# Kernel tuning notes

Hardware: AMD Instinct MI355X
Metric: run time of the kernel (lower is better)

Reference implementation:

```python
import jax, jax.numpy as jnp
import numpy as np

TOP_K = 4  # router top-k


def setup_inputs() -> dict:
    key = jax.random.key(0)
    ks = jax.random.split(key, 8)
    B, S, D, E, H, HS = 2, 2048, 2048, 16, 1024, 4096
    scaled = lambda k, shape, fan: (jax.random.normal(k, shape, jnp.float32) * (fan ** -0.5))
    return {
        "x": jax.random.normal(ks[0], (B, S, D), jnp.float32),
        "w_router": scaled(ks[1], (D, E), D),
        # per-expert SwiGLU MLP weights
        "we1": scaled(ks[2], (E, D, H), D),
        "we3": scaled(ks[3], (E, D, H), D),
        "we2": scaled(ks[4], (E, H, D), H),
        # shared SwiGLU MLP weights
        "ws1": scaled(ks[5], (D, HS), D),
        "ws3": scaled(ks[6], (D, HS), D),
        "ws2": scaled(ks[7], (HS, D), HS),
    }


def reference(x, w_router, we1, we3, we2, ws1, ws3, ws2):
    B, S, D = x.shape
    T = B * S
    E = w_router.shape[1]
    xt = x.reshape(T, D)

    # ---- router: softmax over experts, top-k, renormalize top-k weights ----
    probs = jax.nn.softmax(xt @ w_router, axis=-1)           # [T, E]
    top_w, top_i = jax.lax.top_k(probs, TOP_K)               # [T, K]
    top_w = top_w / jnp.sum(top_w, axis=-1, keepdims=True)
    # dense combine weights [T, E] (zero for non-selected experts)
    cw = jnp.zeros((T, E), xt.dtype).at[jnp.arange(T)[:, None], top_i].add(top_w)

    # ---- experts: per-expert SwiGLU, combine with routing weights ----
    g = jax.nn.silu(jnp.einsum("td,edh->teh", xt, we1)) * jnp.einsum("td,edh->teh", xt, we3)
    g = g * cw[:, :, None]                                   # fold combine weight in
    moe_out = jnp.einsum("teh,ehd->td", g, we2)              # [T, D]

    # ---- shared MLP (SwiGLU) and blend ----
    shared = (jax.nn.silu(xt @ ws1) * (xt @ ws3)) @ ws2      # [T, D]
    k = TOP_K
    out = shared / (k + 1) + moe_out * (k / (k + 1))
    return out.reshape(B, S, D)
```

## Files before the change

kernel.cpp:

```cpp
#include <hip/hip_runtime.h>
#include <stdint.h>

#define TTOK  4096
#define DDIM  2048
#define NEXP  16
#define HDIM  1024
#define HSDIM 4096
#define CAPR  18432

typedef __bf16 bf16x8 __attribute__((ext_vector_type(8)));
typedef float  f32x4  __attribute__((ext_vector_type(4)));

__device__ __forceinline__ unsigned short f2b(float f) {
  union { float f; unsigned int i; } v; v.f = f;
  unsigned int r = (v.i + 0x7fffu + ((v.i >> 16) & 1u)) >> 16;
  return (unsigned short)r;
}
__device__ __forceinline__ float b2f(unsigned short u) {
  union { unsigned int i; float f; } v; v.i = ((unsigned int)u) << 16; return v.f;
}
__device__ __forceinline__ float silu_f(float x) { return x / (1.f + __expf(-x)); }

__device__ __forceinline__ void gload16(const void* g, void* l) {
  __builtin_amdgcn_global_load_lds(
      (const __attribute__((address_space(1))) unsigned int*)(uintptr_t)g,
      (__attribute__((address_space(3))) unsigned int*)(uintptr_t)l,
      16, 0, 0);
}

__device__ __forceinline__ int xcd_swz(int bid, int nwg) {
  int q = nwg >> 3, r = nwg & 7;
  int xcd = bid & 7, off = bid >> 3;
  return (xcd < r ? xcd * (q + 1) : r * (q + 1) + (xcd - r) * q) + off;
}

__global__ void cvt_bf16_kernel(const float* __restrict__ in, unsigned short* __restrict__ out, int n8) {
  int i = blockIdx.x * 256 + threadIdx.x;
  if (i >= n8) return;
  const float4* p = (const float4*)in + (size_t)i * 2;
  float4 a = p[0], b = p[1];
  uint4 o;
  o.x = (unsigned)f2b(a.x) | ((unsigned)f2b(a.y) << 16);
  o.y = (unsigned)f2b(a.z) | ((unsigned)f2b(a.w) << 16);
  o.z = (unsigned)f2b(b.x) | ((unsigned)f2b(b.y) << 16);
  o.w = (unsigned)f2b(b.z) | ((unsigned)f2b(b.w) << 16);
  ((uint4*)out)[i] = o;
}

__global__ void transpose_f2b(const float* __restrict__ in, unsigned short* __restrict__ out, int R, int C) {
  __shared__ unsigned short t[64][66];
  size_t zo = (size_t)blockIdx.z * R * C;
  int c0 = blockIdx.x * 64, r0 = blockIdx.y * 64;
  int x = threadIdx.x & 63, y = threadIdx.x >> 6;
#pragma unroll
  for (int j = 0; j < 16; ++j) {
    int r = y * 16 + j;
    t[x][r] = f2b(in[zo + (size_t)(r0 + r) * C + c0 + x]);
  }
  __syncthreads();
#pragma unroll
  for (int j = 0; j < 16; ++j) {
    int c = y * 16 + j;
    out[zo + (size_t)(c0 + c) * R + r0 + x] = t[c][x];
  }
}

__global__ __launch_bounds__(256) void router_kernel(const float* __restrict__ x, const float* __restrict__ wr,
                                                     float* __restrict__ topw, int* __restrict__ topi) {
  int tok = blockIdx.x * 4 + (threadIdx.x >> 6);
  int lane = threadIdx.x & 63;
  const float* xr = x + (size_t)tok * DDIM;
  float acc[NEXP];
#pragma unroll
  for (int e = 0; e < NEXP; ++e) acc[e] = 0.f;
  for (int it = 0; it < DDIM / 64; ++it) {
    int d = it * 64 + lane;
    float xv = xr[d];
    const float4* w4 = (const float4*)(wr + (size_t)d * NEXP);
    float4 w0 = w4[0], w1 = w4[1], w2 = w4[2], w3 = w4[3];
    acc[0] += xv * w0.x; acc[1] += xv * w0.y; acc[2] += xv * w0.z; acc[3] += xv * w0.w;
    acc[4] += xv * w1.x; acc[5] += xv * w1.y; acc[6] += xv * w1.z; acc[7] += xv * w1.w;
    acc[8] += xv * w2.x; acc[9] += xv * w2.y; acc[10] += xv * w2.z; acc[11] += xv * w2.w;
    acc[12] += xv * w3.x; acc[13] += xv * w3.y; acc[14] += xv * w3.z; acc[15] += xv * w3.w;
  }
#pragma unroll
  for (int e = 0; e < NEXP; ++e) {
#pragma unroll
    for (int off = 32; off > 0; off >>= 1) acc[e] += __shfl_xor(acc[e], off);
  }
  unsigned used = 0u;
  float lv[4]; int si[4];
#pragma unroll
  for (int k = 0; k < 4; ++k) {
    float best = -3.4e38f; int bi = 0;
    for (int e = 0; e < NEXP; ++e) {
      if (!((used >> e) & 1u) && acc[e] > best) { best = acc[e]; bi = e; }
    }
    used |= 1u << bi; lv[k] = best; si[k] = bi;
  }
  if (lane == 0) {
    float m = lv[0], s = 0.f, w[4];
#pragma unroll
    for (int k = 0; k < 4; ++k) { w[k] = __expf(lv[k] - m); s += w[k]; }
    float inv = 1.f / s;
#pragma unroll
    for (int k = 0; k < 4; ++k) { topw[tok * 4 + k] = w[k] * inv; topi[tok * 4 + k] = si[k]; }
  }
}

__global__ void zero_kernel(int* b) { if (threadIdx.x < 64) b[threadIdx.x] = 0; }

__global__ void count_kernel(const int* __restrict__ topi, int* counts, int n) {
  int i = blockIdx.x * 256 + threadIdx.x;
  if (i < n) atomicAdd(&counts[topi[i]], 1);
}

__global__ void offsets_kernel(const int* counts, int* eoff) {
  if (threadIdx.x == 0 && blockIdx.x == 0) {
    int o = 0;
    for (int e = 0; e < NEXP; ++e) { eoff[e] = o; o += (counts[e] + 127) & ~127; }
    eoff[NEXP] = o;
  }
}

__global__ void prefill_kernel(int* gtok, float* gwt, int cap) {
  int i = blockIdx.x * 256 + threadIdx.x;
  if (i < cap) { gtok[i] = 0; gwt[i] = 0.f; }
}

__global__ void scatter_kernel(const int* __restrict__ topi, const float* __restrict__ topw,
                               const int* __restrict__ eoff, int* cursors,
                               int* gtok, float* gwt, int* posmap, int n) {
  int i = blockIdx.x * 256 + threadIdx.x;
  if (i >= n) return;
  int e = topi[i];
  int pos = eoff[e] + atomicAdd(&cursors[e], 1);
  gtok[pos] = i >> 2;
  gwt[pos] = topw[i] * 0.8f;
  posmap[i] = pos;
}

__global__ __launch_bounds__(256) void combine_kernel(const unsigned short* __restrict__ ecout,
                                                      const int* __restrict__ posmap,
                                                      float* __restrict__ out, int n8) {
  int i = blockIdx.x * 256 + threadIdx.x;
  if (i >= n8) return;
  int t = i >> 8;
  int c = i & 255;
  int4 pv = *(const int4*)&posmap[t * 4];
  float s[8];
  float4 o0 = ((const float4*)out)[(size_t)i * 2];
  float4 o1 = ((const float4*)out)[(size_t)i * 2 + 1];
  s[0]=o0.x; s[1]=o0.y; s[2]=o0.z; s[3]=o0.w; s[4]=o1.x; s[5]=o1.y; s[6]=o1.z; s[7]=o1.w;
  int pos[4] = {pv.x, pv.y, pv.z, pv.w};
#pragma unroll
  for (int k = 0; k < 4; ++k) {
    uint4 v = ((const uint4*)(ecout + (size_t)pos[k] * DDIM))[c];
    unsigned* pw = (unsigned*)&v;
#pragma unroll
    for (int w = 0; w < 4; ++w) {
      s[w * 2]     += b2f((unsigned short)(pw[w] & 0xffffu));
      s[w * 2 + 1] += b2f((unsigned short)(pw[w] >> 16));
    }
  }
  float4 r0 = {s[0], s[1], s[2], s[3]}, r1 = {s[4], s[5], s[6], s[7]};
  ((float4*)out)[(size_t)i * 2] = r0;
  ((float4*)out)[(size_t)i * 2 + 1] = r1;
}

template <int MODE>
__global__ __launch_bounds__(512) void gemm_dual(const unsigned short* __restrict__ A,
                                                 const unsigned short* __restrict__ W1,
                                                 const unsigned short* __restrict__ W3,
                                                 unsigned short* __restrict__ G,
                                                 int N, int K, int MB,
                                                 const int* __restrict__ gtok,
                                                 const float* __restrict__ gwt,
                                                 const int* __restrict__ eoff,
                                                 int eBase) {
  __shared__ unsigned short sA[128 * 64];
  __shared__ unsigned short s1[128 * 64];
  __shared__ unsigned short s3[128 * 64];
  __shared__ int sIdx[128];

  int wg = xcd_swz(blockIdx.x, gridDim.x);
  int m0 = (wg % MB) * 128;
  int n0 = (wg / MB) * 128;

  const unsigned short* W1e = W1;
  const unsigned short* W3e = W3;
  if constexpr (MODE == 2) {
    m0 += eoff[eBase];
    if (m0 >= eoff[eBase + 8]) return;
    int e = eBase;
    while (m0 >= eoff[e + 1]) ++e;
    size_t wofs = (size_t)(e - eBase) * N * K;
    W1e += wofs; W3e += wofs;
  }

  int tid = threadIdx.x, lane = tid & 63, wv = tid >> 6;
  if constexpr (MODE == 2) {
    if (tid < 128) sIdx[tid] = gtok[m0 + tid];
    __syncthreads();
  }

  int wm = wv >> 2, wn = wv & 3;
  f32x4 ac1[4][2], ac3[4][2];
#pragma unroll
  for (int mi = 0; mi < 4; ++mi)
#pragma unroll
    for (int ni = 0; ni < 2; ++ni) { ac1[mi][ni] = (f32x4){0,0,0,0}; ac3[mi][ni] = (f32x4){0,0,0,0}; }

  for (int kt = 0; kt < K; kt += 64) {
#pragma unroll
    for (int c = 0; c < 2; ++c) {
      int bofs = (wv * 2 + c) * 1024 + lane * 16;
      int row = bofs >> 7;
      int sch = ((bofs >> 4) & 7) ^ (row & 7);
      int ar;
      if constexpr (MODE == 2) ar = sIdx[row]; else ar = m0 + row;
      gload16(A   + (size_t)ar * K        + kt + sch * 8, &sA[(wv * 2 + c) * 512]);
      gload16(W1e + (size_t)(n0 + row) * K + kt + sch * 8, &s1[(wv * 2 + c) * 512]);
      gload16(W3e + (size_t)(n0 + row) * K + kt + sch * 8, &s3[(wv * 2 + c) * 512]);
    }
    __syncthreads();
#pragma unroll
    for (int kk = 0; kk < 2; ++kk) {
      bf16x8 af[4], b1[2], b3[2];
#pragma unroll
      for (int mi = 0; mi < 4; ++mi) {
        int row = wm * 64 + mi * 16 + (lane & 15);
        int ch = (kk * 4 + (lane >> 4)) ^ (row & 7);
        af[mi] = *(const bf16x8*)&sA[row * 64 + ch * 8];
      }
#pragma unroll
      for (int ni = 0; ni < 2; ++ni) {
        int row = wn * 32 + ni * 16 + (lane & 15);
        int ch = (kk * 4 + (lane >> 4)) ^ (row & 7);
        b1[ni] = *(const bf16x8*)&s1[row * 64 + ch * 8];
        b3[ni] = *(const bf16x8*)&s3[row * 64 + ch * 8];
      }
#pragma unroll
      for (int mi = 0; mi < 4; ++mi)
#pragma unroll
        for (int ni = 0; ni < 2; ++ni) {
          ac1[mi][ni] = __builtin_amdgcn_mfma_f32_16x16x32_bf16(af[mi], b1[ni], ac1[mi][ni], 0, 0, 0);
          ac3[mi][ni] = __builtin_amdgcn_mfma_f32_16x16x32_bf16(af[mi], b3[ni], ac3[mi][ni], 0, 0, 0);
        }
    }
    __syncthreads();
  }

#pragma unroll
  for (int mi = 0; mi < 4; ++mi)
#pragma unroll
    for (int ni = 0; ni < 2; ++ni) {
      int cc = n0 + wn * 32 + ni * 16 + (lane & 15);
#pragma unroll
      for (int j = 0; j < 4; ++j) {
        int rr = m0 + wm * 64 + mi * 16 + ((lane >> 4) << 2) + j;
        float sc;
        if constexpr (MODE == 2) sc = gwt[rr]; else sc = 1.f;
        float g = silu_f(ac1[mi][ni][j]) * ac3[mi][ni][j] * sc;
        G[(size_t)rr * N + cc] = f2b(g);
      }
    }
}

template <int MODE>
__global__ __launch_bounds__(256) void gemm_bt(const unsigned short* __restrict__ A,
                                               const unsigned short* __restrict__ Bt,
                                               unsigned short* __restrict__ Cbf,
                                               float* __restrict__ Cf,
                                               int N, int K, int MB,
                                               const int* __restrict__ eoff,
                                               float scale) {
  __shared__ unsigned short sA[128 * 64];
  __shared__ unsigned short sB[128 * 64];

  int wg = xcd_swz(blockIdx.x, gridDim.x);
  int m0 = (wg % MB) * 128;
  int n0 = (wg / MB) * 128;

  const unsigned short* Bte = Bt;
  if constexpr (MODE == 4) {
    if (m0 >= eoff[NEXP]) return;
    int e = 0;
    while (m0 >= eoff[e + 1]) ++e;
    Bte = Bt + (size_t)e * N * K;
  }
  int tid = threadIdx.x, lane = tid & 63, wv = tid >> 6;
  f32x4 acc[4][4];
#pragma unroll
  for (int mi = 0; mi < 4; ++mi)
#pragma unroll
    for (int ni = 0; ni < 4; ++ni) acc[mi][ni] = (f32x4){0.f, 0.f, 0.f, 0.f};

  int wm = wv >> 1, wn = wv & 1;

  for (int kt = 0; kt < K; kt += 64) {
#pragma unroll
    for (int c = 0; c < 4; ++c) {
      int bofs = (wv * 4 + c) * 1024 + lane * 16;
      int row = bofs >> 7;
      int sch = ((bofs >> 4) & 7) ^ (row & 7);
      gload16(A   + (size_t)(m0 + row) * K + kt + sch * 8, &sA[(wv * 4 + c) * 512]);
      gload16(Bte + (size_t)(n0 + row) * K + kt + sch * 8, &sB[(wv * 4 + c) * 512]);
    }
    __syncthreads();
#pragma unroll
    for (int kk = 0; kk < 2; ++kk) {
      bf16x8 af[4], bfv[4];
#pragma unroll
      for (int mi = 0; mi < 4; ++mi) {
        int row = wm * 64 + mi * 16 + (lane & 15);
        int ch = (kk * 4 + (lane >> 4)) ^ (row & 7);
        af[mi] = *(const bf16x8*)&sA[row * 64 + ch * 8];
      }
#pragma unroll
      for (int ni = 0; ni < 4; ++ni) {
        int row = wn * 64 + ni * 16 + (lane & 15);
        int ch = (kk * 4 + (lane >> 4)) ^ (row & 7);
        bfv[ni] = *(const bf16x8*)&sB[row * 64 + ch * 8];
      }
#pragma unroll
      for (int mi = 0; mi < 4; ++mi)
#pragma unroll
        for (int ni = 0; ni < 4; ++ni)
          acc[mi][ni] = __builtin_amdgcn_mfma_f32_16x16x32_bf16(af[mi], bfv[ni], acc[mi][ni], 0, 0, 0);
    }
    __syncthreads();
  }

#pragma unroll
  for (int mi = 0; mi < 4; ++mi)
#pragma unroll
    for (int ni = 0; ni < 4; ++ni) {
      int cc = n0 + wn * 64 + ni * 16 + (lane & 15);
#pragma unroll
      for (int j = 0; j < 4; ++j) {
        int rr = m0 + wm * 64 + mi * 16 + ((lane >> 4) << 2) + j;
        float v = acc[mi][ni][j];
        if constexpr (MODE == 1) Cf[(size_t)rr * N + cc] = v * scale;
        else Cbf[(size_t)rr * N + cc] = f2b(v);
      }
    }
}

extern "C" void kernel_launch(void* const* d_in, const int* in_sizes, int n_in,
                              void* d_out, int out_size, void* d_ws, size_t ws_size,
                              hipStream_t stream) {
  const float* x   = (const float*)d_in[0];
  const float* wr  = (const float*)d_in[1];
  const float* we1 = (const float*)d_in[2];
  const float* we3 = (const float*)d_in[3];
  const float* we2 = (const float*)d_in[4];
  const float* ws1 = (const float*)d_in[5];
  const float* ws3 = (const float*)d_in[6];
  const float* ws2 = (const float*)d_in[7];
  float* out = (float*)d_out;

  char* p = (char*)d_ws;
  auto take = [&](size_t bytes) { char* r = p; p += (bytes + 255) & ~(size_t)255; return r; };
  unsigned short* xbf   = (unsigned short*)take((size_t)TTOK * DDIM * 2);
  unsigned short* ehg   = (unsigned short*)take((size_t)CAPR * HDIM * 2);
  unsigned short* gsh   = (unsigned short*)take((size_t)TTOK * HSDIM * 2);
  unsigned short* ecout = (unsigned short*)take((size_t)CAPR * DDIM * 2);
  unsigned short* twArena = (unsigned short*)take((size_t)NEXP * HDIM * DDIM * 2);
  float* topw = (float*)take((size_t)TTOK * 4 * 4);
  int*   topi = (int*)take((size_t)TTOK * 4 * 4);
  int*   gtok = (int*)take((size_t)CAPR * 4);
  float* gwt  = (float*)take((size_t)CAPR * 4);
  int*   posmap = (int*)take((size_t)TTOK * 4 * 4);
  int*   ibuf = (int*)take(256);
  if ((size_t)(p - (char*)d_ws) > ws_size) return;

  unsigned short* twA = twArena;
  unsigned short* twB = twArena + (size_t)8 * DDIM * HDIM;

  int* counts  = ibuf;
  int* cursors = ibuf + 16;
  int* eoff    = ibuf + 32;

  cvt_bf16_kernel<<<TTOK * DDIM / 8 / 256, 256, 0, stream>>>(x, xbf, TTOK * DDIM / 8);
  router_kernel<<<TTOK / 4, 256, 0, stream>>>(x, wr, topw, topi);
  zero_kernel<<<1, 64, 0, stream>>>(ibuf);
  count_kernel<<<TTOK * 4 / 256, 256, 0, stream>>>(topi, counts, TTOK * 4);
  offsets_kernel<<<1, 64, 0, stream>>>(counts, eoff);
  prefill_kernel<<<CAPR / 256, 256, 0, stream>>>(gtok, gwt, CAPR);
  scatter_kernel<<<TTOK * 4 / 256, 256, 0, stream>>>(topi, topw, eoff, cursors, gtok, gwt, posmap, TTOK * 4);

  transpose_f2b<<<dim3(HSDIM / 64, DDIM / 64, 1), 256, 0, stream>>>(ws1, twA, DDIM, HSDIM);
  transpose_f2b<<<dim3(HSDIM / 64, DDIM / 64, 1), 256, 0, stream>>>(ws3, twB, DDIM, HSDIM);
  gemm_dual<0><<<(TTOK / 128) * (HSDIM / 128), 512, 0, stream>>>(xbf, twA, twB, gsh, HSDIM, DDIM,
                                                                 TTOK / 128, nullptr, nullptr, nullptr, 0);
  transpose_f2b<<<dim3(DDIM / 64, HSDIM / 64, 1), 256, 0, stream>>>(ws2, twA, HSDIM, DDIM);
  gemm_bt<1><<<(TTOK / 128) * (DDIM / 128), 256, 0, stream>>>(gsh, twA, nullptr, out, DDIM, HSDIM,
                                                              TTOK / 128, nullptr, 0.2f);

  for (int h = 0; h < 2; ++h) {
    const float* w1h = we1 + (size_t)h * 8 * DDIM * HDIM;
    const float* w3h = we3 + (size_t)h * 8 * DDIM * HDIM;
    transpose_f2b<<<dim3(HDIM / 64, DDIM / 64, 8), 256, 0, stream>>>(w1h, twA, DDIM, HDIM);
    transpose_f2b<<<dim3(HDIM / 64, DDIM / 64, 8), 256, 0, stream>>>(w3h, twB, DDIM, HDIM);
    gemm_dual<2><<<(CAPR / 128) * (HDIM / 128), 512, 0, stream>>>(xbf, twA, twB, ehg, HDIM, DDIM,
                                                                  CAPR / 128, gtok, gwt, eoff, 8 * h);
  }
  transpose_f2b<<<dim3(DDIM / 64, HDIM / 64, NEXP), 256, 0, stream>>>(we2, twArena, HDIM, DDIM);
  gemm_bt<4><<<(CAPR / 128) * (DDIM / 128), 256, 0, stream>>>(ehg, twArena, ecout, nullptr, DDIM, HDIM,
                                                              CAPR / 128, eoff, 0.f);

  combine_kernel<<<TTOK * DDIM / 8 / 256, 256, 0, stream>>>(ecout, posmap, out, TTOK * DDIM / 8);
}
```

Baseline: 820.5 us.

## Vectorize weight transpose, widen gemm_bt tiles, run all experts in one pass

The fp32-to-bf16 weight transpose now uses float4 loads and ushort4 stores instead of scalar accesses. The down-projection GEMM grows to 128x256 tiles with 8 waves per block, so each block reuses its A tile across twice as many output columns. The expert gate/up projection now runs once over all 16 experts, keeping the transposed we3 in the shared-MLP gsh buffer instead of two half passes. This cuts launches and lets one grid cover every expert, but it needs more LDS per block and depends on gsh being large enough and no longer in use.

```diff
diff --git a/kernel.cpp b/kernel.cpp
--- a/kernel.cpp
+++ b/kernel.cpp
@@ -47,21 +47,29 @@
   ((uint4*)out)[i] = o;
 }
 
-__global__ void transpose_f2b(const float* __restrict__ in, unsigned short* __restrict__ out, int R, int C) {
-  __shared__ unsigned short t[64][66];
-  size_t zo = (size_t)blockIdx.z * R * C;
+__global__ __launch_bounds__(256) void transpose_f2b(const float* __restrict__ in,
+                                                     unsigned short* __restrict__ out, int R, int C) {
+  __shared__ unsigned short t[64][68];
+  size_t zo = (size_t)blockIdx.z * (size_t)R * C;
   int c0 = blockIdx.x * 64, r0 = blockIdx.y * 64;
-  int x = threadIdx.x & 63, y = threadIdx.x >> 6;
-#pragma unroll
-  for (int j = 0; j < 16; ++j) {
-    int r = y * 16 + j;
-    t[x][r] = f2b(in[zo + (size_t)(r0 + r) * C + c0 + x]);
+  int tid = threadIdx.x;
+#pragma unroll
+  for (int p = 0; p < 4; ++p) {
+    int id = p * 256 + tid;
+    int r = id >> 4;
+    int c4 = (id & 15) * 4;
+    float4 v = *(const float4*)&in[zo + (size_t)(r0 + r) * C + c0 + c4];
+    ushort4 w = { f2b(v.x), f2b(v.y), f2b(v.z), f2b(v.w) };
+    *(ushort4*)&t[r][c4] = w;
   }
   __syncthreads();
 #pragma unroll
-  for (int j = 0; j < 16; ++j) {
-    int c = y * 16 + j;
-    out[zo + (size_t)(c0 + c) * R + r0 + x] = t[c][x];
+  for (int p = 0; p < 4; ++p) {
+    int id = p * 256 + tid;
+    int c = id >> 4;
+    int r4 = (id & 15) * 4;
+    ushort4 w = { t[r4][c], t[r4 + 1][c], t[r4 + 2][c], t[r4 + 3][c] };
+    *(ushort4*)&out[zo + (size_t)(c0 + c) * R + r0 + r4] = w;
   }
 }
 
@@ -168,7 +176,7 @@
   ((float4*)out)[(size_t)i * 2 + 1] = r1;
 }
 
-template <int MODE>
+template <int MODE, int ESPAN>
 __global__ __launch_bounds__(512) void gemm_dual(const unsigned short* __restrict__ A,
                                                  const unsigned short* __restrict__ W1,
                                                  const unsigned short* __restrict__ W3,
@@ -191,7 +199,7 @@
   const unsigned short* W3e = W3;
   if constexpr (MODE == 2) {
     m0 += eoff[eBase];
-    if (m0 >= eoff[eBase + 8]) return;
+    if (m0 >= eoff[eBase + ESPAN]) return;
     int e = eBase;
     while (m0 >= eoff[e + 1]) ++e;
     size_t wofs = (size_t)(e - eBase) * N * K;
@@ -268,19 +276,19 @@
 }
 
 template <int MODE>
-__global__ __launch_bounds__(256) void gemm_bt(const unsigned short* __restrict__ A,
-                                               const unsigned short* __restrict__ Bt,
-                                               unsigned short* __restrict__ Cbf,
-                                               float* __restrict__ Cf,
-                                               int N, int K, int MB,
-                                               const int* __restrict__ eoff,
-                                               float scale) {
+__global__ __launch_bounds__(512) void gemm_bt8(const unsigned short* __restrict__ A,
+                                                const unsigned short* __restrict__ Bt,
+                                                unsigned short* __restrict__ Cbf,
+                                                float* __restrict__ Cf,
+                                                int N, int K, int MB,
+                                                const int* __restrict__ eoff,
+                                                float scale) {
   __shared__ unsigned short sA[128 * 64];
-  __shared__ unsigned short sB[128 * 64];
+  __shared__ unsigned short sB[256 * 64];
 
   int wg = xcd_swz(blockIdx.x, gridDim.x);
   int m0 = (wg % MB) * 128;
-  int n0 = (wg / MB) * 128;
+  int n0 = (wg / MB) * 256;
 
   const unsigned short* Bte = Bt;
   if constexpr (MODE == 4) {
@@ -290,21 +298,26 @@
     Bte = Bt + (size_t)e * N * K;
   }
   int tid = threadIdx.x, lane = tid & 63, wv = tid >> 6;
+  int wm = wv >> 2, wn = wv & 3;
   f32x4 acc[4][4];
 #pragma unroll
   for (int mi = 0; mi < 4; ++mi)
 #pragma unroll
     for (int ni = 0; ni < 4; ++ni) acc[mi][ni] = (f32x4){0.f, 0.f, 0.f, 0.f};
 
-  int wm = wv >> 1, wn = wv & 1;
-
   for (int kt = 0; kt < K; kt += 64) {
+#pragma unroll
+    for (int c = 0; c < 2; ++c) {
+      int bofs = (wv * 2 + c) * 1024 + lane * 16;
+      int row = bofs >> 7;
+      int sch = ((bofs >> 4) & 7) ^ (row & 7);
+      gload16(A + (size_t)(m0 + row) * K + kt + sch * 8, &sA[(wv * 2 + c) * 512]);
+    }
 #pragma unroll
     for (int c = 0; c < 4; ++c) {
       int bofs = (wv * 4 + c) * 1024 + lane * 16;
       int row = bofs >> 7;
       int sch = ((bofs >> 4) & 7) ^ (row & 7);
-      gload16(A   + (size_t)(m0 + row) * K + kt + sch * 8, &sA[(wv * 4 + c) * 512]);
       gload16(Bte + (size_t)(n0 + row) * K + kt + sch * 8, &sB[(wv * 4 + c) * 512]);
     }
     __syncthreads();
@@ -377,6 +390,7 @@
 
   unsigned short* twA = twArena;
   unsigned short* twB = twArena + (size_t)8 * DDIM * HDIM;
+  unsigned short* we3t = gsh;
 
   int* counts  = ibuf;
   int* cursors = ibuf + 16;
@@ -392,23 +406,19 @@
 
   transpose_f2b<<<dim3(HSDIM / 64, DDIM / 64, 1), 256, 0, stream>>>(ws1, twA, DDIM, HSDIM);
   transpose_f2b<<<dim3(HSDIM / 64, DDIM / 64, 1), 256, 0, stream>>>(ws3, twB, DDIM, HSDIM);
-  gemm_dual<0><<<(TTOK / 128) * (HSDIM / 128), 512, 0, stream>>>(xbf, twA, twB, gsh, HSDIM, DDIM,
-                                                                 TTOK / 128, nullptr, nullptr, nullptr, 0);
+  gemm_dual<0, NEXP><<<(TTOK / 128) * (HSDIM / 128), 512, 0, stream>>>(xbf, twA, twB, gsh, HSDIM, DDIM,
+                                                                       TTOK / 128, nullptr, nullptr, nullptr, 0);
   transpose_f2b<<<dim3(DDIM / 64, HSDIM / 64, 1), 256, 0, stream>>>(ws2, twA, HSDIM, DDIM);
-  gemm_bt<1><<<(TTOK / 128) * (DDIM / 128), 256, 0, stream>>>(gsh, twA, nullptr, out, DDIM, HSDIM,
-                                                              TTOK / 128, nullptr, 0.2f);
-
-  for (int h = 0; h < 2; ++h) {
-    const float* w1h = we1 + (size_t)h * 8 * DDIM * HDIM;
-    const float* w3h = we3 + (size_t)h * 8 * DDIM * HDIM;
-    transpose_f2b<<<dim3(HDIM / 64, DDIM / 64, 8), 256, 0, stream>>>(w1h, twA, DDIM, HDIM);
-    transpose_f2b<<<dim3(HDIM / 64, DDIM / 64, 8), 256, 0, stream>>>(w3h, twB, DDIM, HDIM);
-    gemm_dual<2><<<(CAPR / 128) * (HDIM / 128), 512, 0, stream>>>(xbf, twA, twB, ehg, HDIM, DDIM,
-                                                                  CAPR / 128, gtok, gwt, eoff, 8 * h);
-  }
+  gemm_bt8<1><<<(TTOK / 128) * (DDIM / 256), 512, 0, stream>>>(gsh, twA, nullptr, out, DDIM, HSDIM,
+                                                               TTOK / 128, nullptr, 0.2f);
+
+  transpose_f2b<<<dim3(HDIM / 64, DDIM / 64, NEXP), 256, 0, stream>>>(we1, twArena, DDIM, HDIM);
+  transpose_f2b<<<dim3(HDIM / 64, DDIM / 64, NEXP), 256, 0, stream>>>(we3, we3t, DDIM, HDIM);
+  gemm_dual<2, NEXP><<<(CAPR / 128) * (HDIM / 128), 512, 0, stream>>>(xbf, twArena, we3t, ehg, HDIM, DDIM,
+                                                                      CAPR / 128, gtok, gwt, eoff, 0);
   transpose_f2b<<<dim3(DDIM / 64, HDIM / 64, NEXP), 256, 0, stream>>>(we2, twArena, HDIM, DDIM);
-  gemm_bt<4><<<(CAPR / 128) * (DDIM / 128), 256, 0, stream>>>(ehg, twArena, ecout, nullptr, DDIM, HDIM,
-                                                              CAPR / 128, eoff, 0.f);
+  gemm_bt8<4><<<(CAPR / 128) * (DDIM / 256), 512, 0, stream>>>(ehg, twArena, ecout, nullptr, DDIM, HDIM,
+                                                               CAPR / 128, eoff, 0.f);
 
   combine_kernel<<<TTOK * DDIM / 8 / 256, 256, 0, stream>>>(ecout, posmap, out, TTOK * DDIM / 8);
 }
```

Result: faster. 796.8 us (-2.9%).
